# Performance work log

Hardware: AMD Instinct MI355X
Metric: run time of the kernel (lower is better)

Reference implementation:

```python
import jax, jax.numpy as jnp
import numpy as np

T, B, V, H, L = 512, 256, 128, 256, 2


def _lstm_layer(x, h0, c0, Wih, Whh, bih, bhh):
    """Single LSTM layer. x: [T,B,Din]. Returns ys [T,B,H], (h,c) [B,H]."""
    # Input projection for all timesteps at once: [T,B,4H]
    xg = jnp.einsum('tbd,gd->tbg', x, Wih) + bih + bhh

    def step(carry, xg_t):
        h, c = carry
        g = xg_t + h @ Whh.T                      # [B,4H]
        i, f, gg, o = jnp.split(g, 4, axis=-1)    # PyTorch gate order i,f,g,o
        i = jax.nn.sigmoid(i)
        f = jax.nn.sigmoid(f)
        gg = jnp.tanh(gg)
        o = jax.nn.sigmoid(o)
        c = f * c + i * gg
        h = o * jnp.tanh(c)
        return (h, c), h

    (h, c), ys = jax.lax.scan(step, (h0, c0), xg)
    return ys, h, c


def setup_inputs() -> dict:
    key = jax.random.key(0)
    ks = jax.random.split(key, 12)
    s_in = 1.0 / np.sqrt(H)  # PyTorch LSTM init: U(-1/sqrt(H), 1/sqrt(H))
    u = lambda k, shape, s: jax.random.uniform(k, shape, jnp.float32, -s, s)
    return {
        'x': jax.random.normal(ks[0], (T, B, V), jnp.float32),
        'h0': jnp.zeros((L, B, H), jnp.float32),
        'c0': jnp.zeros((L, B, H), jnp.float32),
        'Wih0': u(ks[1], (4 * H, V), s_in),
        'Whh0': u(ks[2], (4 * H, H), s_in),
        'bih0': u(ks[3], (4 * H,), s_in),
        'bhh0': u(ks[4], (4 * H,), s_in),
        'Wih1': u(ks[5], (4 * H, H), s_in),
        'Whh1': u(ks[6], (4 * H, H), s_in),
        'bih1': u(ks[7], (4 * H,), s_in),
        'bhh1': u(ks[8], (4 * H,), s_in),
        'Wfc': jax.random.uniform(ks[9], (V, H), jnp.float32, -1.0, 1.0),
        'bfc': jnp.zeros((V,), jnp.float32),
    }


def reference(x, h0, c0, Wih0, Whh0, bih0, bhh0, Wih1, Whh1, bih1, bhh1, Wfc, bfc):
    # Layer 0
    y0, h_0, c_0 = _lstm_layer(x, h0[0], c0[0], Wih0, Whh0, bih0, bhh0)
    # Inter-layer dropout and post-LSTM dropout are identity in eval mode.
    # Layer 1
    y1, h_1, c_1 = _lstm_layer(y0, h0[1], c0[1], Wih1, Whh1, bih1, bhh1)
    hidden = jnp.stack([h_0, h_1])  # [2,B,H]
    cell = jnp.stack([c_0, c_1])
    # Flatten and project: [T*B, V]
    out = y1.reshape(T * B, H) @ Wfc.T + bfc
    return out, hidden, cell
```

## Files before the change

### kernel.cpp

```cpp
#include <hip/hip_runtime.h>
#include <hip/hip_bf16.h>

#define DI __device__ __forceinline__

typedef short bf16x8 __attribute__((ext_vector_type(8)));
typedef float f32x4 __attribute__((ext_vector_type(4)));
typedef int   i32x4 __attribute__((ext_vector_type(4)));
typedef unsigned short u16;

constexpr int TT = 512, BB = 256, HH = 256, VV = 128;

DI u16 f2b(float f){ __hip_bfloat16 h = __float2bfloat16(f); u16 r; __builtin_memcpy(&r,&h,2); return r; }
DI float b2f(u16 v){ unsigned u = ((unsigned)v)<<16; float f; __builtin_memcpy(&f,&u,4); return f; }
DI f32x4 mfma16(bf16x8 a, bf16x8 b, f32x4 c){ return __builtin_amdgcn_mfma_f32_16x16x32_bf16(a,b,c,0,0,0); }

__global__ void pack_b(const float* __restrict__ W, u16* __restrict__ o, int N, int K){
  const int tid = blockIdx.x*256 + threadIdx.x;
  const int KT = K >> 5;
  const int total = (N>>4)*KT*64;
  if (tid >= total) return;
  const int lane = tid & 63;
  const int rest = tid >> 6;
  const int kt  = rest % KT;
  const int ntg = rest / KT;
  const int n  = (ntg<<4) + (lane&15);
  const int k0 = (kt<<5) + ((lane>>4)<<3);
  const float* s = W + (size_t)n*K + k0;
  bf16x8 pv;
#pragma unroll
  for (int j=0;j<8;++j) pv[j] = (short)f2b(s[j]);
  *(bf16x8*)(o + (size_t)tid*8) = pv;
}

__global__ void bias_sum(const float* a0,const float* b0,float* o0,
                         const float* a1,const float* b1,float* o1){
  int i = blockIdx.x*256 + threadIdx.x;
  if (i < 1024) o0[i] = a0[i] + b0[i];
  else if (i < 2048) { int j=i-1024; o1[j] = a1[j] + b1[j]; }
}

template<int KT, bool AF32>
DI void gemm_body(char* smem, const void* __restrict__ A_,
                  const u16* __restrict__ Bp, const float* __restrict__ bias,
                  u16* __restrict__ xgp, int lda, int bx, int by)
{
  constexpr int NT = 8;
  const int tid = threadIdx.x;
  const int l = tid & 63, w = tid >> 6;
  const int l15 = l & 15, g4 = l >> 4;
  const int mw = w >> 1, nw = w & 1;
  const int col0 = bx * 256;
  const int row0 = by * 64;

  {
    const int n16 = 2*NT*KT*64;
    const i32x4* src = (const i32x4*)(Bp + (size_t)(col0>>4)*KT*64*8);
    i32x4* dst = (i32x4*)smem;
    for (int i=tid; i<n16; i+=512) dst[i] = src[i];
  }
  __syncthreads();

  f32x4 acc[NT];
#pragma unroll
  for (int nt=0; nt<NT; ++nt) acc[nt] = (f32x4){0.f,0.f,0.f,0.f};

  const int rowA = row0 + mw*16 + l15;
#pragma unroll
  for (int kt=0; kt<KT; ++kt){
    bf16x8 a;
    const int k0 = kt*32 + g4*8;
    if constexpr (AF32){
      const float* ap = (const float*)A_ + (size_t)rowA*lda + k0;
      const f32x4 x0 = *(const f32x4*)ap;
      const f32x4 x1 = *(const f32x4*)(ap+4);
#pragma unroll
      for (int j=0;j<4;++j){ a[j] = (short)f2b(x0[j]); a[j+4] = (short)f2b(x1[j]); }
    } else {
      a = *(const bf16x8*)((const u16*)A_ + (size_t)rowA*lda + k0);
    }
#pragma unroll
    for (int nt=0; nt<NT; ++nt){
      const bf16x8 b = *(const bf16x8*)(smem + (size_t)(((nw*NT+nt)*KT + kt)*64 + l)*16);
      acc[nt] = mfma16(a,b,acc[nt]);
    }
  }

  const int t  = row0 >> 8;
  const int bg = ((row0 & 255) >> 4) + mw;
#pragma unroll
  for (int j=0;j<4;++j){
    bf16x8 pk;
#pragma unroll
    for (int p=0;p<2;++p){
      const int nt = 2*j + p;
      const float bv = bias[col0 + (nw*8+nt)*16 + l15];
#pragma unroll
      for (int i=0;i<4;++i) pk[p*4+i] = (short)f2b(acc[nt][i] + bv);
    }
    const int wr = nw*4 + j;
    *(bf16x8*)(xgp + ((((size_t)(t*4 + bx)*16 + bg)*8 + wr)*64 + l)*8) = pk;
  }
}

__global__ __launch_bounds__(512,2) void gemm_perm0(const float* A, const u16* Bp,
    const float* bias, u16* xgp){
  __shared__ char smem[65536];
  gemm_body<4,true>(smem, A, Bp, bias, xgp, VV, blockIdx.x, blockIdx.y);
}

DI void fc_body(char* smem, const u16* __restrict__ A_,
                const u16* __restrict__ Bp, const float* __restrict__ bias,
                float* __restrict__ C_, int by)
{
  constexpr int KT = 8, NT = 4;
  const int tid = threadIdx.x;
  const int l = tid & 63, w = tid >> 6;
  const int l15 = l & 15, g4 = l >> 4;
  const int mw = w >> 1, nw = w & 1;
  const int row0 = by * 64;

  {
    const int n16 = 2*NT*KT*64;
    const i32x4* src = (const i32x4*)Bp;
    i32x4* dst = (i32x4*)smem;
    for (int i=tid; i<n16; i+=512) dst[i] = src[i];
  }
  __syncthreads();

  f32x4 acc[NT];
#pragma unroll
  for (int nt=0; nt<NT; ++nt) acc[nt] = (f32x4){0.f,0.f,0.f,0.f};

  const int rowA = row0 + mw*16 + l15;
#pragma unroll
  for (int kt=0; kt<KT; ++kt){
    const bf16x8 a = *(const bf16x8*)(A_ + (size_t)rowA*HH + kt*32 + g4*8);
#pragma unroll
    for (int nt=0; nt<NT; ++nt){
      const bf16x8 b = *(const bf16x8*)(smem + (size_t)(((nw*NT+nt)*KT + kt)*64 + l)*16);
      acc[nt] = mfma16(a,b,acc[nt]);
    }
  }

  __syncthreads();

#pragma unroll
  for (int nt=0; nt<NT; ++nt){
    const int col = (nw*NT+nt)*16 + l15;
    const float bv = bias[col];
#pragma unroll
    for (int i=0;i<4;++i)
      C_[(size_t)(row0 + mw*16 + 4*g4 + i)*VV + col] = acc[nt][i] + bv;
  }
}

DI void rec_body(char* smW, char* smH0, char* smH1,
    const u16* __restrict__ xg, const u16* __restrict__ Whhp,
    const float* h_in, const float* c_in, u16* __restrict__ y,
    float* hout, float* cout, int bg, int nsteps)
{
  const int tid = threadIdx.x;
  const int w = tid >> 6, l = tid & 63;
  const int l15 = l & 15, g4 = l >> 4;
  const int b0 = bg * 16;

  const u16* xt = xg + ((size_t)(bg*8 + w)*64 + l)*8;
  const int yb = tid >> 5;
  const int yj = (tid & 31) * 8;

  bf16x8 xsv[4];
#pragma unroll
  for (int q=0;q<4;++q) xsv[q] = *(const bf16x8*)(xt + q*65536);

  bf16x8 Wr[4][8];
#pragma unroll
  for (int nt=0; nt<4; ++nt){
    const int ntg = ((nt>>1)<<4) + (w<<1) + (nt&1);
#pragma unroll
    for (int kt=0; kt<8; ++kt)
      Wr[nt][kt] = *(const bf16x8*)(Whhp + (((size_t)ntg*8 + kt)*64 + l)*8);
  }
#pragma unroll
  for (int ntl=0; ntl<2; ++ntl){
    const int ntg = 48 + (w<<1) + ntl;
#pragma unroll
    for (int kt=0; kt<8; ++kt){
      bf16x8 v = *(const bf16x8*)(Whhp + (((size_t)ntg*8 + kt)*64 + l)*8);
      *(bf16x8*)(smW + (size_t)((w*16 + ntl*8 + kt)*64 + l)*16) = v;
    }
  }
  const u16* wg0 = Whhp + (((size_t)(32 + 2*w)*8)*64 + l)*8;
  const u16* wg1 = Whhp + (((size_t)(33 + 2*w)*8)*64 + l)*8;
  bf16x8 p00 = *(const bf16x8*)(wg0);
  bf16x8 p01 = *(const bf16x8*)(wg0 + 512);
  bf16x8 p10 = *(const bf16x8*)(wg1);
  bf16x8 p11 = *(const bf16x8*)(wg1 + 512);

  float c[2][4];
#pragma unroll
  for (int hf=0; hf<2; ++hf)
#pragma unroll
    for (int i=0;i<4;++i){
      const int b  = 4*g4 + i;
      const int jh = 32*w + 16*hf + l15;
      c[hf][i] = c_in[(size_t)(b0+b)*256 + jh];
      *(u16*)(smH0 + (size_t)b*528 + 2*jh) = f2b(h_in[(size_t)(b0+b)*256 + jh]);
    }
  __syncthreads();

  for (int t = 0; t < nsteps; ++t) {
    const char* hrd = (t&1) ? smH1 : smH0;
    char*       hwr = (t&1) ? smH0 : smH1;

    if (t){
      const bf16x8 hv = *(const bf16x8*)(hrd + (size_t)yb*528 + yj*2);
      *(bf16x8*)(y + ((size_t)(t-1)*256 + b0 + yb)*256 + yj) = hv;
    }

    bf16x8 gA[8], gB[8];
    gA[0]=p00; gA[1]=p01; gB[0]=p10; gB[1]=p11;

    gA[2] = *(const bf16x8*)(wg0 + 2*512);
    gB[2] = *(const bf16x8*)(wg1 + 2*512);
    const bf16x8 a0 = *(const bf16x8*)(hrd + (size_t)l15*528 + g4*16);
    f32x4 acc[8];
#pragma unroll
    for (int nt=0; nt<4; ++nt){
      f32x4 x0;
#pragma unroll
      for (int i=0;i<4;++i) x0[i] = b2f((u16)xsv[nt>>1][(nt&1)*4+i]);
      acc[nt] = mfma16(a0, Wr[nt][0], x0);
    }
    {
      f32x4 x4, x5;
#pragma unroll
      for (int i=0;i<4;++i){ x4[i] = b2f((u16)xsv[2][i]); x5[i] = b2f((u16)xsv[2][4+i]); }
      acc[4] = mfma16(a0, gA[0], x4);
      acc[5] = mfma16(a0, gB[0], x5);
    }
#pragma unroll
    for (int ntl=0; ntl<2; ++ntl){
      const int nt = 6+ntl;
      f32x4 x0;
#pragma unroll
      for (int i=0;i<4;++i) x0[i] = b2f((u16)xsv[3][ntl*4+i]);
      const bf16x8 wl = *(const bf16x8*)(smW + (size_t)((w*16 + ntl*8)*64 + l)*16);
      acc[nt] = mfma16(a0, wl, x0);
    }
    xt += 262144;
#pragma unroll
    for (int q=0;q<4;++q) xsv[q] = *(const bf16x8*)(xt + q*65536);

#pragma unroll
    for (int kt=1; kt<8; ++kt){
      if (kt < 6){
        gA[kt+2] = *(const bf16x8*)(wg0 + (size_t)(kt+2)*512);
        gB[kt+2] = *(const bf16x8*)(wg1 + (size_t)(kt+2)*512);
      }
      const bf16x8 a = *(const bf16x8*)(hrd + (size_t)l15*528 + kt*64 + g4*16);
#pragma unroll
      for (int nt=0; nt<4; ++nt) acc[nt] = mfma16(a, Wr[nt][kt], acc[nt]);
      acc[4] = mfma16(a, gA[kt], acc[4]);
      acc[5] = mfma16(a, gB[kt], acc[5]);
#pragma unroll
      for (int ntl=0; ntl<2; ++ntl){
        const bf16x8 wl = *(const bf16x8*)(smW + (size_t)((w*16 + ntl*8 + kt)*64 + l)*16);
        acc[6+ntl] = mfma16(a, wl, acc[6+ntl]);
      }
    }

    p00 = *(const bf16x8*)(wg0);
    p01 = *(const bf16x8*)(wg0 + 512);
    p10 = *(const bf16x8*)(wg1);
    p11 = *(const bf16x8*)(wg1 + 512);

#pragma unroll
    for (int hf=0; hf<2; ++hf){
#pragma unroll
      for (int i=0;i<4;++i){
        const float xi = acc[0+hf][i];
        const float xf = acc[2+hf][i];
        const float xG = acc[4+hf][i];
        const float xo = acc[6+hf][i];
        const float ai = __builtin_amdgcn_exp2f(-1.4426950408889634f*xi);
        const float af = __builtin_amdgcn_exp2f(-1.4426950408889634f*xf);
        const float bg = __builtin_amdgcn_exp2f(-2.8853900817779268f*xG);
        const float rig = __builtin_amdgcn_rcpf((1.0f+ai)*(1.0f+bg));
        const float rf  = __builtin_amdgcn_rcpf(1.0f+af);
        const float cc  = c[hf][i]*rf + (1.0f-bg)*rig;
        c[hf][i] = cc;
        const float ao = __builtin_amdgcn_exp2f(-1.4426950408889634f*xo);
        const float dc = __builtin_amdgcn_exp2f(-2.8853900817779268f*cc);
        const float roc = __builtin_amdgcn_rcpf((1.0f+ao)*(1.0f+dc));
        const float hh  = (1.0f-dc)*roc;
        *(u16*)(hwr + (size_t)(4*g4+i)*528 + 2*(32*w + 16*hf + l15)) = f2b(hh);
      }
    }
    __syncthreads();
  }

  {
    const bf16x8 hv = *(const bf16x8*)(smH0 + (size_t)yb*528 + yj*2);
    *(bf16x8*)(y + ((size_t)(nsteps-1)*256 + b0 + yb)*256 + yj) = hv;
  }
#pragma unroll
  for (int hf=0; hf<2; ++hf)
#pragma unroll
    for (int i=0;i<4;++i){
      const int b  = 4*g4 + i;
      const int jh = 32*w + 16*hf + l15;
      hout[(size_t)(b0+b)*256 + jh] = b2f(*(u16*)(smH0 + (size_t)b*528 + 2*jh));
      cout[(size_t)(b0+b)*256 + jh] = c[hf][i];
    }
}

__global__ __launch_bounds__(512,2) void mega(
    int hasR0, int hasR1, int hasG0, int hasG1, int hasFC, int nsteps,
    const u16* __restrict__ xg0r, const float* hinA, const float* cinA,
    u16* y0wr, float* houtA, float* coutA,
    const u16* __restrict__ xg1r, const float* hinB, const float* cinB,
    u16* y1wr, float* houtB, float* coutB,
    const float* __restrict__ xG0, u16* __restrict__ xg0w,
    const u16* __restrict__ y0rd, u16* __restrict__ xg1w,
    const u16* __restrict__ y1fc, float* __restrict__ outfc,
    const u16* __restrict__ wih0p, const float* __restrict__ bias0,
    const u16* __restrict__ wih1p, const float* __restrict__ bias1,
    const u16* __restrict__ whh0p, const u16* __restrict__ whh1p,
    const u16* __restrict__ wfcp,  const float* __restrict__ bfc)
{
  __shared__ char smem[147968];
  const int bid = (int)blockIdx.x;
  const int ntG = nsteps * 16;

  if (bid < 16){
    if (hasR0)
      rec_body(smem, smem+131072, smem+131072+8448, xg0r, whh0p,
               hinA, cinA, y0wr, houtA, coutA, bid, nsteps);
  } else if (bid < 32){
    if (hasR1)
      rec_body(smem, smem+131072, smem+131072+8448, xg1r, whh1p,
               hinB, cinB, y1wr, houtB, coutB, bid-16, nsteps);
  } else {
    const int gb = bid - 32;
    if (hasG0){
      for (int tile = gb; tile < ntG; tile += 224){
        gemm_body<4,true >(smem, xG0, wih0p, bias0, xg0w, VV, tile&3, tile>>2);
        __syncthreads();
      }
    }
    if (hasG1){
      for (int tile = gb; tile < ntG; tile += 224){
        gemm_body<8,false>(smem, y0rd, wih1p, bias1, xg1w, HH, tile&3, tile>>2);
        __syncthreads();
      }
    }
    if (hasFC){
      for (int tile = gb; tile < nsteps*4; tile += 224){
        fc_body(smem, y1fc, wfcp, bfc, outfc, tile);
        __syncthreads();
      }
    }
  }
}

extern "C" void kernel_launch(void* const* d_in, const int* in_sizes, int n_in,
                              void* d_out, int out_size, void* d_ws, size_t ws_size,
                              hipStream_t stream) {
  (void)in_sizes; (void)n_in; (void)out_size;
  const float* x    = (const float*)d_in[0];
  const float* h0   = (const float*)d_in[1];
  const float* c0   = (const float*)d_in[2];
  const float* Wih0 = (const float*)d_in[3];
  const float* Whh0 = (const float*)d_in[4];
  const float* bih0 = (const float*)d_in[5];
  const float* bhh0 = (const float*)d_in[6];
  const float* Wih1 = (const float*)d_in[7];
  const float* Whh1 = (const float*)d_in[8];
  const float* bih1 = (const float*)d_in[9];
  const float* bhh1 = (const float*)d_in[10];
  const float* Wfc  = (const float*)d_in[11];
  const float* bfc  = (const float*)d_in[12];
  float* out = (float*)d_out;

  const int TCr  = (ws_size >= (size_t)82*1024*1024) ? 32 : 16;
  const int NCHr = TT / TCr;
  const size_t XGB = (size_t)TCr*BB*1024*2 + 524288;
  const size_t Y0B = (size_t)TCr*BB*HH*2;

  char* p = (char*)d_ws;
  u16* xg0b[2]; u16* xg1b[2]; u16* y0b[2];
  xg0b[0] = (u16*)p; p += XGB;
  xg0b[1] = (u16*)p; p += XGB;
  xg1b[0] = (u16*)p; p += XGB;
  xg1b[1] = (u16*)p; p += XGB;
  y0b[0]  = (u16*)p; p += Y0B;
  y0b[1]  = (u16*)p; p += Y0B;
  u16* whh0p = (u16*)p; p += 524288;
  u16* whh1p = (u16*)p; p += 524288;
  u16* wih0p = (u16*)p; p += 262144;
  u16* wih1p = (u16*)p; p += 524288;
  u16* wfcp  = (u16*)p; p += 65536;
  float* bias0 = (float*)p; p += 4096;
  float* bias1 = (float*)p; p += 4096;
  float* hst0 = (float*)p; p += 262144;
  float* cst0 = (float*)p; p += 262144;
  float* hst1 = (float*)p; p += 262144;
  float* cst1 = (float*)p; p += 262144;

  u16* y1    = (u16*)d_out;
  float* hid = out + 16777216;
  float* cel = hid + 131072;

  pack_b<<<64 ,256,0,stream>>>(Wih0, wih0p, 1024,128);
  pack_b<<<128,256,0,stream>>>(Whh0, whh0p, 1024,256);
  pack_b<<<128,256,0,stream>>>(Wih1, wih1p, 1024,256);
  pack_b<<<128,256,0,stream>>>(Whh1, whh1p, 1024,256);
  pack_b<<<16 ,256,0,stream>>>(Wfc,  wfcp,  128,256);
  bias_sum<<<8,256,0,stream>>>(bih0,bhh0,bias0, bih1,bhh1,bias1);

  gemm_perm0<<<dim3(4, TCr*4),512,0,stream>>>(x, wih0p, bias0, xg0b[0]);

  for (int d = 0; d <= NCHr + 2; ++d){
    const int hasR0 = (d < NCHr);
    const int hasR1 = (d >= 2) && (d < NCHr + 2);
    const int hasG0 = (d + 1 < NCHr);
    const int hasG1 = (d >= 1) && (d - 1 < NCHr);
    const int hasFC = (d >= 3) && (d - 3 < NCHr);
    const int cR1 = hasR1 ? d-2 : 0;
    const int cG0 = hasG0 ? d+1 : 0;
    const int cFC = hasFC ? d-3 : 0;
    mega<<<256,512,0,stream>>>(
      hasR0, hasR1, hasG0, hasG1, hasFC, TCr,
      xg0b[d&1],
      (d==0) ? h0 : hst0, (d==0) ? c0 : cst0,
      y0b[d&1],
      (d==NCHr-1) ? hid : hst0, (d==NCHr-1) ? cel : cst0,
      xg1b[d&1],
      (cR1==0) ? (h0+65536) : hst1, (cR1==0) ? (c0+65536) : cst1,
      y1 + (size_t)cR1*TCr*BB*HH,
      (cR1==NCHr-1) ? (hid+65536) : hst1, (cR1==NCHr-1) ? (cel+65536) : cst1,
      x + (size_t)cG0*TCr*BB*VV, xg0b[(d+1)&1],
      y0b[(d-1)&1], xg1b[(d-1)&1],
      y1 + (size_t)cFC*TCr*BB*HH, out + (size_t)cFC*TCr*BB*VV,
      wih0p, bias0, wih1p, bias1, whh0p, whh1p, wfcp, bfc);
  }
}
```

Baseline: 1.629 ms.

## Stream output-gate Whh from global and write y directly from registers

The output-gate weight tiles in the recurrent body were staged in LDS. They are now streamed from global/L2 each step, alongside the g-gate tiles, with the first two k-slices held in registers. The y output is written per element straight from the activation epilogue, replacing the separate vectorized copy from LDS at the start of the next step. This takes LDS reads off the serial step path and drops one LDS read of h per step, at the cost of more global load traffic, more registers and scattered 2-byte global stores.

```diff
diff --git a/kernel.cpp b/kernel.cpp
--- a/kernel.cpp
+++ b/kernel.cpp
@@ -154,7 +154,7 @@
   }
 }
 
-DI void rec_body(char* smW, char* smH0, char* smH1,
+DI void rec_body(char* smH0, char* smH1,
     const u16* __restrict__ xg, const u16* __restrict__ Whhp,
     const float* h_in, const float* c_in, u16* __restrict__ y,
     float* hout, float* cout, int bg, int nsteps)
@@ -165,8 +165,7 @@
   const int b0 = bg * 16;
 
   const u16* xt = xg + ((size_t)(bg*8 + w)*64 + l)*8;
-  const int yb = tid >> 5;
-  const int yj = (tid & 31) * 8;
+  u16* yp = y + (size_t)(b0 + 4*g4)*256 + 32*w + l15;
 
   bf16x8 xsv[4];
 #pragma unroll
@@ -180,21 +179,18 @@
     for (int kt=0; kt<8; ++kt)
       Wr[nt][kt] = *(const bf16x8*)(Whhp + (((size_t)ntg*8 + kt)*64 + l)*8);
   }
-#pragma unroll
-  for (int ntl=0; ntl<2; ++ntl){
-    const int ntg = 48 + (w<<1) + ntl;
-#pragma unroll
-    for (int kt=0; kt<8; ++kt){
-      bf16x8 v = *(const bf16x8*)(Whhp + (((size_t)ntg*8 + kt)*64 + l)*8);
-      *(bf16x8*)(smW + (size_t)((w*16 + ntl*8 + kt)*64 + l)*16) = v;
-    }
-  }
   const u16* wg0 = Whhp + (((size_t)(32 + 2*w)*8)*64 + l)*8;
   const u16* wg1 = Whhp + (((size_t)(33 + 2*w)*8)*64 + l)*8;
-  bf16x8 p00 = *(const bf16x8*)(wg0);
-  bf16x8 p01 = *(const bf16x8*)(wg0 + 512);
-  bf16x8 p10 = *(const bf16x8*)(wg1);
-  bf16x8 p11 = *(const bf16x8*)(wg1 + 512);
+  const u16* wo0 = Whhp + (((size_t)(48 + 2*w)*8)*64 + l)*8;
+  const u16* wo1 = Whhp + (((size_t)(49 + 2*w)*8)*64 + l)*8;
+  const bf16x8 p00 = *(const bf16x8*)(wg0);
+  const bf16x8 p01 = *(const bf16x8*)(wg0 + 512);
+  const bf16x8 p10 = *(const bf16x8*)(wg1);
+  const bf16x8 p11 = *(const bf16x8*)(wg1 + 512);
+  const bf16x8 q00 = *(const bf16x8*)(wo0);
+  const bf16x8 q01 = *(const bf16x8*)(wo0 + 512);
+  const bf16x8 q10 = *(const bf16x8*)(wo1);
+  const bf16x8 q11 = *(const bf16x8*)(wo1 + 512);
 
   float c[2][4];
 #pragma unroll
@@ -212,16 +208,14 @@
     const char* hrd = (t&1) ? smH1 : smH0;
     char*       hwr = (t&1) ? smH0 : smH1;
 
-    if (t){
-      const bf16x8 hv = *(const bf16x8*)(hrd + (size_t)yb*528 + yj*2);
-      *(bf16x8*)(y + ((size_t)(t-1)*256 + b0 + yb)*256 + yj) = hv;
-    }
-
-    bf16x8 gA[8], gB[8];
+    bf16x8 gA[8], gB[8], oA[8], oB[8];
     gA[0]=p00; gA[1]=p01; gB[0]=p10; gB[1]=p11;
-
-    gA[2] = *(const bf16x8*)(wg0 + 2*512);
-    gB[2] = *(const bf16x8*)(wg1 + 2*512);
+    oA[0]=q00; oA[1]=q01; oB[0]=q10; oB[1]=q11;
+
+    gA[2] = *(const bf16x8*)(wg0 + 1024);
+    gB[2] = *(const bf16x8*)(wg1 + 1024);
+    oA[2] = *(const bf16x8*)(wo0 + 1024);
+    oB[2] = *(const bf16x8*)(wo1 + 1024);
     const bf16x8 a0 = *(const bf16x8*)(hrd + (size_t)l15*528 + g4*16);
     f32x4 acc[8];
 #pragma unroll
@@ -232,20 +226,16 @@
       acc[nt] = mfma16(a0, Wr[nt][0], x0);
     }
     {
-      f32x4 x4, x5;
-#pragma unroll
-      for (int i=0;i<4;++i){ x4[i] = b2f((u16)xsv[2][i]); x5[i] = b2f((u16)xsv[2][4+i]); }
+      f32x4 x4, x5, x6, x7;
+#pragma unroll
+      for (int i=0;i<4;++i){
+        x4[i] = b2f((u16)xsv[2][i]);   x5[i] = b2f((u16)xsv[2][4+i]);
+        x6[i] = b2f((u16)xsv[3][i]);   x7[i] = b2f((u16)xsv[3][4+i]);
+      }
       acc[4] = mfma16(a0, gA[0], x4);
       acc[5] = mfma16(a0, gB[0], x5);
-    }
-#pragma unroll
-    for (int ntl=0; ntl<2; ++ntl){
-      const int nt = 6+ntl;
-      f32x4 x0;
-#pragma unroll
-      for (int i=0;i<4;++i) x0[i] = b2f((u16)xsv[3][ntl*4+i]);
-      const bf16x8 wl = *(const bf16x8*)(smW + (size_t)((w*16 + ntl*8)*64 + l)*16);
-      acc[nt] = mfma16(a0, wl, x0);
+      acc[6] = mfma16(a0, oA[0], x6);
+      acc[7] = mfma16(a0, oB[0], x7);
     }
     xt += 262144;
 #pragma unroll
@@ -256,23 +246,17 @@
       if (kt < 6){
         gA[kt+2] = *(const bf16x8*)(wg0 + (size_t)(kt+2)*512);
         gB[kt+2] = *(const bf16x8*)(wg1 + (size_t)(kt+2)*512);
+        oA[kt+2] = *(const bf16x8*)(wo0 + (size_t)(kt+2)*512);
+        oB[kt+2] = *(const bf16x8*)(wo1 + (size_t)(kt+2)*512);
       }
       const bf16x8 a = *(const bf16x8*)(hrd + (size_t)l15*528 + kt*64 + g4*16);
 #pragma unroll
       for (int nt=0; nt<4; ++nt) acc[nt] = mfma16(a, Wr[nt][kt], acc[nt]);
       acc[4] = mfma16(a, gA[kt], acc[4]);
       acc[5] = mfma16(a, gB[kt], acc[5]);
-#pragma unroll
-      for (int ntl=0; ntl<2; ++ntl){
-        const bf16x8 wl = *(const bf16x8*)(smW + (size_t)((w*16 + ntl*8 + kt)*64 + l)*16);
-        acc[6+ntl] = mfma16(a, wl, acc[6+ntl]);
-      }
-    }
-
-    p00 = *(const bf16x8*)(wg0);
-    p01 = *(const bf16x8*)(wg0 + 512);
-    p10 = *(const bf16x8*)(wg1);
-    p11 = *(const bf16x8*)(wg1 + 512);
+      acc[6] = mfma16(a, oA[kt], acc[6]);
+      acc[7] = mfma16(a, oB[kt], acc[7]);
+    }
 
 #pragma unroll
     for (int hf=0; hf<2; ++hf){
@@ -284,25 +268,24 @@
         const float xo = acc[6+hf][i];
         const float ai = __builtin_amdgcn_exp2f(-1.4426950408889634f*xi);
         const float af = __builtin_amdgcn_exp2f(-1.4426950408889634f*xf);
-        const float bg = __builtin_amdgcn_exp2f(-2.8853900817779268f*xG);
-        const float rig = __builtin_amdgcn_rcpf((1.0f+ai)*(1.0f+bg));
+        const float eg = __builtin_amdgcn_exp2f(-2.8853900817779268f*xG);
+        const float rig = __builtin_amdgcn_rcpf((1.0f+ai)*(1.0f+eg));
         const float rf  = __builtin_amdgcn_rcpf(1.0f+af);
-        const float cc  = c[hf][i]*rf + (1.0f-bg)*rig;
+        const float cc  = c[hf][i]*rf + (1.0f-eg)*rig;
         c[hf][i] = cc;
         const float ao = __builtin_amdgcn_exp2f(-1.4426950408889634f*xo);
         const float dc = __builtin_amdgcn_exp2f(-2.8853900817779268f*cc);
         const float roc = __builtin_amdgcn_rcpf((1.0f+ao)*(1.0f+dc));
         const float hh  = (1.0f-dc)*roc;
-        *(u16*)(hwr + (size_t)(4*g4+i)*528 + 2*(32*w + 16*hf + l15)) = f2b(hh);
-      }
-    }
+        const u16 hb = f2b(hh);
+        *(u16*)(hwr + (size_t)(4*g4+i)*528 + 2*(32*w + 16*hf + l15)) = hb;
+        yp[(size_t)i*256 + hf*16] = hb;
+      }
+    }
+    yp += 65536;
     __syncthreads();
   }
 
-  {
-    const bf16x8 hv = *(const bf16x8*)(smH0 + (size_t)yb*528 + yj*2);
-    *(bf16x8*)(y + ((size_t)(nsteps-1)*256 + b0 + yb)*256 + yj) = hv;
-  }
 #pragma unroll
   for (int hf=0; hf<2; ++hf)
 #pragma unroll
@@ -334,11 +317,11 @@
 
   if (bid < 16){
     if (hasR0)
-      rec_body(smem, smem+131072, smem+131072+8448, xg0r, whh0p,
+      rec_body(smem+131072, smem+131072+8448, xg0r, whh0p,
                hinA, cinA, y0wr, houtA, coutA, bid, nsteps);
   } else if (bid < 32){
     if (hasR1)
-      rec_body(smem, smem+131072, smem+131072+8448, xg1r, whh1p,
+      rec_body(smem+131072, smem+131072+8448, xg1r, whh1p,
                hinB, cinB, y1wr, houtB, coutB, bid-16, nsteps);
   } else {
     const int gb = bid - 32;
```

Result: slower. 2.807 ms (+72.3%).

## Replace per-step block barrier with per-wave flags and triple-buffered hidden state

Applied to the files above, without the earlier changes.

The recurrent loop drops the __syncthreads at the end of each timestep. Each wave now publishes a workgroup-scope release flag after writing its slice of h, and the other waves spin on those flags one k-chunk at a time. Each wave starts its k-loop at its own chunk and rotates through the rest, so it can begin before every other wave has finished. A third hidden-state buffer guards against write-after-read hazards, and y is written straight from registers instead of being reread from shared memory. The aim is to cut barrier stalls on the serial critical path, at the cost of spin-polling, larger shared memory, and a bailout counter that could hide ordering bugs.

```diff
diff --git a/kernel.cpp b/kernel.cpp
--- a/kernel.cpp
+++ b/kernel.cpp
@@ -154,19 +154,20 @@
   }
 }
 
-DI void rec_body(char* smW, char* smH0, char* smH1,
+DI void rec_body(char* smW, char* bA, char* bB, char* bC, int* flg,
     const u16* __restrict__ xg, const u16* __restrict__ Whhp,
     const float* h_in, const float* c_in, u16* __restrict__ y,
     float* hout, float* cout, int bg, int nsteps)
 {
   const int tid = threadIdx.x;
-  const int w = tid >> 6, l = tid & 63;
+  const int w0 = tid >> 6, l = tid & 63;
   const int l15 = l & 15, g4 = l >> 4;
   const int b0 = bg * 16;
 
-  const u16* xt = xg + ((size_t)(bg*8 + w)*64 + l)*8;
-  const int yb = tid >> 5;
-  const int yj = (tid & 31) * 8;
+  if (tid < 8) flg[tid] = -1;
+
+  const u16* xt = xg + ((size_t)(bg*8 + w0)*64 + l)*8;
+  u16* yp = y + (size_t)(b0 + 4*g4)*256 + 32*w0 + l15;
 
   bf16x8 xsv[4];
 #pragma unroll
@@ -175,26 +176,28 @@
   bf16x8 Wr[4][8];
 #pragma unroll
   for (int nt=0; nt<4; ++nt){
-    const int ntg = ((nt>>1)<<4) + (w<<1) + (nt&1);
-#pragma unroll
-    for (int kt=0; kt<8; ++kt)
-      Wr[nt][kt] = *(const bf16x8*)(Whhp + (((size_t)ntg*8 + kt)*64 + l)*8);
+    const int ntg = ((nt>>1)<<4) + (w0<<1) + (nt&1);
+#pragma unroll
+    for (int j=0; j<8; ++j){
+      const int kt = (w0 + j) & 7;
+      Wr[nt][j] = *(const bf16x8*)(Whhp + (((size_t)ntg*8 + kt)*64 + l)*8);
+    }
   }
 #pragma unroll
   for (int ntl=0; ntl<2; ++ntl){
-    const int ntg = 48 + (w<<1) + ntl;
+    const int ntg = 48 + (w0<<1) + ntl;
 #pragma unroll
     for (int kt=0; kt<8; ++kt){
       bf16x8 v = *(const bf16x8*)(Whhp + (((size_t)ntg*8 + kt)*64 + l)*8);
-      *(bf16x8*)(smW + (size_t)((w*16 + ntl*8 + kt)*64 + l)*16) = v;
-    }
-  }
-  const u16* wg0 = Whhp + (((size_t)(32 + 2*w)*8)*64 + l)*8;
-  const u16* wg1 = Whhp + (((size_t)(33 + 2*w)*8)*64 + l)*8;
-  bf16x8 p00 = *(const bf16x8*)(wg0);
-  bf16x8 p01 = *(const bf16x8*)(wg0 + 512);
-  bf16x8 p10 = *(const bf16x8*)(wg1);
-  bf16x8 p11 = *(const bf16x8*)(wg1 + 512);
+      *(bf16x8*)(smW + (size_t)((w0*16 + ntl*8 + kt)*64 + l)*16) = v;
+    }
+  }
+  const u16* wg0 = Whhp + (((size_t)(32 + 2*w0)*8)*64 + l)*8;
+  const u16* wg1 = Whhp + (((size_t)(33 + 2*w0)*8)*64 + l)*8;
+  const bf16x8 p00 = *(const bf16x8*)(wg0 + (size_t)( w0      & 7)*512);
+  const bf16x8 p01 = *(const bf16x8*)(wg0 + (size_t)((w0 + 1) & 7)*512);
+  const bf16x8 p10 = *(const bf16x8*)(wg1 + (size_t)( w0      & 7)*512);
+  const bf16x8 p11 = *(const bf16x8*)(wg1 + (size_t)((w0 + 1) & 7)*512);
 
   float c[2][4];
 #pragma unroll
@@ -202,80 +205,75 @@
 #pragma unroll
     for (int i=0;i<4;++i){
       const int b  = 4*g4 + i;
-      const int jh = 32*w + 16*hf + l15;
+      const int jh = 32*w0 + 16*hf + l15;
       c[hf][i] = c_in[(size_t)(b0+b)*256 + jh];
-      *(u16*)(smH0 + (size_t)b*528 + 2*jh) = f2b(h_in[(size_t)(b0+b)*256 + jh]);
+      *(u16*)(bA + (size_t)b*528 + 2*jh) = f2b(h_in[(size_t)(b0+b)*256 + jh]);
     }
   __syncthreads();
 
+  char* br = bA; char* bw = bB; char* bn = bC;
+
   for (int t = 0; t < nsteps; ++t) {
-    const char* hrd = (t&1) ? smH1 : smH0;
-    char*       hwr = (t&1) ? smH0 : smH1;
-
-    if (t){
-      const bf16x8 hv = *(const bf16x8*)(hrd + (size_t)yb*528 + yj*2);
-      *(bf16x8*)(y + ((size_t)(t-1)*256 + b0 + yb)*256 + yj) = hv;
-    }
-
     bf16x8 gA[8], gB[8];
     gA[0]=p00; gA[1]=p01; gB[0]=p10; gB[1]=p11;
-
-    gA[2] = *(const bf16x8*)(wg0 + 2*512);
-    gB[2] = *(const bf16x8*)(wg1 + 2*512);
-    const bf16x8 a0 = *(const bf16x8*)(hrd + (size_t)l15*528 + g4*16);
     f32x4 acc[8];
-#pragma unroll
-    for (int nt=0; nt<4; ++nt){
-      f32x4 x0;
-#pragma unroll
-      for (int i=0;i<4;++i) x0[i] = b2f((u16)xsv[nt>>1][(nt&1)*4+i]);
-      acc[nt] = mfma16(a0, Wr[nt][0], x0);
-    }
-    {
-      f32x4 x4, x5;
-#pragma unroll
-      for (int i=0;i<4;++i){ x4[i] = b2f((u16)xsv[2][i]); x5[i] = b2f((u16)xsv[2][4+i]); }
-      acc[4] = mfma16(a0, gA[0], x4);
-      acc[5] = mfma16(a0, gB[0], x5);
-    }
-#pragma unroll
-    for (int ntl=0; ntl<2; ++ntl){
-      const int nt = 6+ntl;
-      f32x4 x0;
-#pragma unroll
-      for (int i=0;i<4;++i) x0[i] = b2f((u16)xsv[3][ntl*4+i]);
-      const bf16x8 wl = *(const bf16x8*)(smW + (size_t)((w*16 + ntl*8)*64 + l)*16);
-      acc[nt] = mfma16(a0, wl, x0);
-    }
-    xt += 262144;
-#pragma unroll
-    for (int q=0;q<4;++q) xsv[q] = *(const bf16x8*)(xt + q*65536);
-
-#pragma unroll
-    for (int kt=1; kt<8; ++kt){
-      if (kt < 6){
-        gA[kt+2] = *(const bf16x8*)(wg0 + (size_t)(kt+2)*512);
-        gB[kt+2] = *(const bf16x8*)(wg1 + (size_t)(kt+2)*512);
-      }
-      const bf16x8 a = *(const bf16x8*)(hrd + (size_t)l15*528 + kt*64 + g4*16);
-#pragma unroll
-      for (int nt=0; nt<4; ++nt) acc[nt] = mfma16(a, Wr[nt][kt], acc[nt]);
-      acc[4] = mfma16(a, gA[kt], acc[4]);
-      acc[5] = mfma16(a, gB[kt], acc[5]);
-#pragma unroll
-      for (int ntl=0; ntl<2; ++ntl){
-        const bf16x8 wl = *(const bf16x8*)(smW + (size_t)((w*16 + ntl*8 + kt)*64 + l)*16);
-        acc[6+ntl] = mfma16(a, wl, acc[6+ntl]);
-      }
-    }
-
-    p00 = *(const bf16x8*)(wg0);
-    p01 = *(const bf16x8*)(wg0 + 512);
-    p10 = *(const bf16x8*)(wg1);
-    p11 = *(const bf16x8*)(wg1 + 512);
-
-#pragma unroll
-    for (int hf=0; hf<2; ++hf){
+
+#pragma unroll
+    for (int j=0; j<8; ++j){
+      const int kt = (w0 + j) & 7;
+      if (j){
+        int bail = 0;
+        for (;;){
+          const int f = __hip_atomic_load(&flg[kt], __ATOMIC_ACQUIRE,
+                                          __HIP_MEMORY_SCOPE_WORKGROUP);
+          if (f >= t-1 || ++bail > (1<<22)) break;
+          __builtin_amdgcn_s_sleep(1);
+        }
+      }
+      const bf16x8 a = *(const bf16x8*)(br + (size_t)l15*528 + kt*64 + g4*16);
+      if (j == 0){
+        f32x4 xv[8];
+#pragma unroll
+        for (int nt=0; nt<4; ++nt)
+#pragma unroll
+          for (int i=0;i<4;++i) xv[nt][i] = b2f((u16)xsv[nt>>1][(nt&1)*4+i]);
+#pragma unroll
+        for (int i=0;i<4;++i){
+          xv[4][i] = b2f((u16)xsv[2][i]);   xv[5][i] = b2f((u16)xsv[2][4+i]);
+          xv[6][i] = b2f((u16)xsv[3][i]);   xv[7][i] = b2f((u16)xsv[3][4+i]);
+        }
+#pragma unroll
+        for (int nt=0; nt<4; ++nt) acc[nt] = mfma16(a, Wr[nt][0], xv[nt]);
+        acc[4] = mfma16(a, gA[0], xv[4]);
+        acc[5] = mfma16(a, gB[0], xv[5]);
+        {
+          const bf16x8 wl0 = *(const bf16x8*)(smW + (size_t)((w0*16 +      kt)*64 + l)*16);
+          const bf16x8 wl1 = *(const bf16x8*)(smW + (size_t)((w0*16 + 8 +  kt)*64 + l)*16);
+          acc[6] = mfma16(a, wl0, xv[6]);
+          acc[7] = mfma16(a, wl1, xv[7]);
+        }
+        xt += 262144;
+#pragma unroll
+        for (int q=0;q<4;++q) xsv[q] = *(const bf16x8*)(xt + q*65536);
+      } else {
+#pragma unroll
+        for (int nt=0; nt<4; ++nt) acc[nt] = mfma16(a, Wr[nt][j], acc[nt]);
+        acc[4] = mfma16(a, gA[j], acc[4]);
+        acc[5] = mfma16(a, gB[j], acc[5]);
+        const bf16x8 wl0 = *(const bf16x8*)(smW + (size_t)((w0*16 +      kt)*64 + l)*16);
+        const bf16x8 wl1 = *(const bf16x8*)(smW + (size_t)((w0*16 + 8 +  kt)*64 + l)*16);
+        acc[6] = mfma16(a, wl0, acc[6]);
+        acc[7] = mfma16(a, wl1, acc[7]);
+      }
+      if (j < 6){
+        gA[j+2] = *(const bf16x8*)(wg0 + (size_t)((w0 + j + 2) & 7)*512);
+        gB[j+2] = *(const bf16x8*)(wg1 + (size_t)((w0 + j + 2) & 7)*512);
+      }
+    }
+
+    u16 hb[8];
+#pragma unroll
+    for (int hf=0; hf<2; ++hf)
 #pragma unroll
       for (int i=0;i<4;++i){
         const float xi = acc[0+hf][i];
@@ -284,32 +282,38 @@
         const float xo = acc[6+hf][i];
         const float ai = __builtin_amdgcn_exp2f(-1.4426950408889634f*xi);
         const float af = __builtin_amdgcn_exp2f(-1.4426950408889634f*xf);
-        const float bg = __builtin_amdgcn_exp2f(-2.8853900817779268f*xG);
-        const float rig = __builtin_amdgcn_rcpf((1.0f+ai)*(1.0f+bg));
+        const float eg = __builtin_amdgcn_exp2f(-2.8853900817779268f*xG);
+        const float rig = __builtin_amdgcn_rcpf((1.0f+ai)*(1.0f+eg));
         const float rf  = __builtin_amdgcn_rcpf(1.0f+af);
-        const float cc  = c[hf][i]*rf + (1.0f-bg)*rig;
+        const float cc  = c[hf][i]*rf + (1.0f-eg)*rig;
         c[hf][i] = cc;
         const float ao = __builtin_amdgcn_exp2f(-1.4426950408889634f*xo);
         const float dc = __builtin_amdgcn_exp2f(-2.8853900817779268f*cc);
         const float roc = __builtin_amdgcn_rcpf((1.0f+ao)*(1.0f+dc));
         const float hh  = (1.0f-dc)*roc;
-        *(u16*)(hwr + (size_t)(4*g4+i)*528 + 2*(32*w + 16*hf + l15)) = f2b(hh);
-      }
-    }
-    __syncthreads();
-  }
-
-  {
-    const bf16x8 hv = *(const bf16x8*)(smH0 + (size_t)yb*528 + yj*2);
-    *(bf16x8*)(y + ((size_t)(nsteps-1)*256 + b0 + yb)*256 + yj) = hv;
-  }
+        hb[hf*4+i] = f2b(hh);
+        *(u16*)(bw + (size_t)(4*g4+i)*528 + 2*(32*w0 + 16*hf + l15)) = hb[hf*4+i];
+      }
+
+    __hip_atomic_store(&flg[w0], t, __ATOMIC_RELEASE, __HIP_MEMORY_SCOPE_WORKGROUP);
+
+#pragma unroll
+    for (int hf=0; hf<2; ++hf)
+#pragma unroll
+      for (int i=0;i<4;++i)
+        yp[(size_t)i*256 + hf*16] = hb[hf*4+i];
+    yp += 65536;
+
+    { char* t0 = br; br = bw; bw = bn; bn = t0; }
+  }
+
 #pragma unroll
   for (int hf=0; hf<2; ++hf)
 #pragma unroll
     for (int i=0;i<4;++i){
       const int b  = 4*g4 + i;
-      const int jh = 32*w + 16*hf + l15;
-      hout[(size_t)(b0+b)*256 + jh] = b2f(*(u16*)(smH0 + (size_t)b*528 + 2*jh));
+      const int jh = 32*w0 + 16*hf + l15;
+      hout[(size_t)(b0+b)*256 + jh] = b2f(*(u16*)(br + (size_t)b*528 + 2*jh));
       cout[(size_t)(b0+b)*256 + jh] = c[hf][i];
     }
 }
@@ -328,17 +332,18 @@
     const u16* __restrict__ whh0p, const u16* __restrict__ whh1p,
     const u16* __restrict__ wfcp,  const float* __restrict__ bfc)
 {
-  __shared__ char smem[147968];
+  __shared__ char smem[156416];
+  __shared__ int  flgS[8];
   const int bid = (int)blockIdx.x;
   const int ntG = nsteps * 16;
 
   if (bid < 16){
     if (hasR0)
-      rec_body(smem, smem+131072, smem+131072+8448, xg0r, whh0p,
+      rec_body(smem, smem+131072, smem+139520, smem+147968, flgS, xg0r, whh0p,
                hinA, cinA, y0wr, houtA, coutA, bid, nsteps);
   } else if (bid < 32){
     if (hasR1)
-      rec_body(smem, smem+131072, smem+131072+8448, xg1r, whh1p,
+      rec_body(smem, smem+131072, smem+139520, smem+147968, flgS, xg1r, whh1p,
                hinB, cinB, y1wr, houtB, coutB, bid-16, nsteps);
   } else {
     const int gb = bid - 32;
```

Result: slower. 2.849 ms (+74.8%).
